# Optimization experiments

Measured on AMD Instinct MI355X. Metric: run time of the kernel, lower is better.

## Reference

```python
import jax, jax.numpy as jnp
import numpy as np

EPS = 1e-5
PDIM, QKD, DIM = 64, 16, 256
SCALE = QKD ** -0.5


def setup_inputs() -> dict:
    key = jax.random.key(0)
    ks = jax.random.split(key, 13)
    B, H, W = 8, 64, 64
    return {
        "x": jax.random.normal(ks[0], (B, DIM, H, W), jnp.float32),
        "gn_g": jax.random.uniform(ks[1], (PDIM,), jnp.float32, 0.5, 1.5),
        "gn_b": jax.random.normal(ks[2], (PDIM,), jnp.float32) * 0.1,
        "qkv_w": jax.random.normal(ks[3], (2 * QKD + PDIM, PDIM), jnp.float32) * (PDIM ** -0.5),
        "qkv_bn_g": jax.random.uniform(ks[4], (2 * QKD + PDIM,), jnp.float32, 0.5, 1.5),
        "qkv_bn_b": jax.random.normal(ks[5], (2 * QKD + PDIM,), jnp.float32) * 0.1,
        "qkv_rm": jax.random.normal(ks[6], (2 * QKD + PDIM,), jnp.float32) * 0.1,
        "qkv_rv": jax.random.uniform(ks[7], (2 * QKD + PDIM,), jnp.float32, 0.5, 1.5),
        "proj_w": jax.random.normal(ks[8], (DIM, DIM), jnp.float32) * (DIM ** -0.5),
        "proj_bn_g": jax.random.uniform(ks[9], (DIM,), jnp.float32, 0.5, 1.5),
        "proj_bn_b": jax.random.normal(ks[10], (DIM,), jnp.float32) * 0.1,
        "proj_rm": jax.random.normal(ks[11], (DIM,), jnp.float32) * 0.1,
        "proj_rv": jax.random.uniform(ks[12], (DIM,), jnp.float32, 0.5, 1.5),
    }


def _bn(y, g, b, rm, rv):
    # inference BatchNorm over channel axis 1 of [B,C,H,W]
    inv = g / jnp.sqrt(rv + EPS)
    return y * inv[None, :, None, None] + (b - rm * inv)[None, :, None, None]


def reference(x, gn_g, gn_b, qkv_w, qkv_bn_g, qkv_bn_b, qkv_rm, qkv_rv,
              proj_w, proj_bn_g, proj_bn_b, proj_rm, proj_rv):
    B, C, H, W = x.shape
    x1, x2 = x[:, :PDIM], x[:, PDIM:]
    # GroupNorm with 1 group: normalize over (C,H,W) per sample
    mu = jnp.mean(x1, axis=(1, 2, 3), keepdims=True)
    var = jnp.var(x1, axis=(1, 2, 3), keepdims=True)
    x1n = (x1 - mu) / jnp.sqrt(var + EPS)
    x1n = x1n * gn_g[None, :, None, None] + gn_b[None, :, None, None]
    # qkv: 1x1 conv + BN
    qkv = jnp.einsum('bchw,oc->bohw', x1n, qkv_w)
    qkv = _bn(qkv, qkv_bn_g, qkv_bn_b, qkv_rm, qkv_rv)
    q, k, v = qkv[:, :QKD], qkv[:, QKD:2 * QKD], qkv[:, 2 * QKD:]
    N = H * W
    q = q.reshape(B, QKD, N)
    k = k.reshape(B, QKD, N)
    v = v.reshape(B, PDIM, N)
    attn = jnp.einsum('bcn,bcm->bnm', q, k) * SCALE  # [B,N,N]
    attn = jax.nn.softmax(attn, axis=-1)
    x1_attn = jnp.einsum('bcm,bnm->bcn', v, attn).reshape(B, PDIM, H, W)
    xc = jnp.concatenate([x1_attn, x2], axis=1)
    # proj: ReLU -> 1x1 conv -> BN
    y = jnp.einsum('bchw,oc->bohw', jax.nn.relu(xc), proj_w)
    return _bn(y, proj_bn_g, proj_bn_b, proj_rm, proj_rv)
```

## Files before the change

### kernel.cpp

```cpp
#include <hip/hip_runtime.h>
#include <hip/hip_bf16.h>

typedef __bf16 bf16;
typedef __bf16 bf16x4 __attribute__((ext_vector_type(4)));
typedef __bf16 bf16x8 __attribute__((ext_vector_type(8)));
typedef float  f32x16 __attribute__((ext_vector_type(16)));

#define MFMA32 __builtin_amdgcn_mfma_f32_32x32x16_bf16
#define EPSV 1e-5f
#define QSCALE 0.36067376022224085f

__device__ __forceinline__ f32x16 fzero16() {
  f32x16 z;
#pragma unroll
  for (int i = 0; i < 16; ++i) z[i] = 0.f;
  return z;
}

__global__ __launch_bounds__(256) void k_stats_partial(const float* __restrict__ x,
                                                       float* __restrict__ part) {
  const int b = blockIdx.x >> 5, k = blockIdx.x & 31;
  const float* p = x + (size_t)b * 256 * 4096 + k * 8192;
  const int t = threadIdx.x;
  float s = 0.f, q = 0.f;
#pragma unroll
  for (int j = 0; j < 8; ++j) {
    float4 v = ((const float4*)p)[t + j * 256];
    s += v.x + v.y + v.z + v.w;
    q += v.x * v.x + v.y * v.y + v.z * v.z + v.w * v.w;
  }
  __shared__ float ls[256], lq[256];
  ls[t] = s; lq[t] = q;
  __syncthreads();
  for (int off = 128; off > 0; off >>= 1) {
    if (t < off) { ls[t] += ls[t + off]; lq[t] += lq[t + off]; }
    __syncthreads();
  }
  if (t == 0) { part[blockIdx.x * 2] = ls[0]; part[blockIdx.x * 2 + 1] = lq[0]; }
}

__global__ __launch_bounds__(256) void k_stats_final(const float* __restrict__ part,
                                                     float* __restrict__ stats) {
  const int t = threadIdx.x, b = t >> 5, k = t & 31;
  float s = part[(b * 32 + k) * 2], q = part[(b * 32 + k) * 2 + 1];
  for (int off = 16; off > 0; off >>= 1) {
    s += __shfl_down(s, off, 32);
    q += __shfl_down(q, off, 32);
  }
  if (k == 0) {
    const float inv_n = 1.f / 262144.f;
    const float mu = s * inv_n;
    const float var = q * inv_n - mu * mu;
    stats[b * 2] = mu;
    stats[b * 2 + 1] = rsqrtf(var + EPSV);
  }
}

__global__ __launch_bounds__(256) void k_qkv(
    const float* __restrict__ x, const float* __restrict__ gn_g, const float* __restrict__ gn_b,
    const float* __restrict__ qkv_w, const float* __restrict__ bn_g, const float* __restrict__ bn_b,
    const float* __restrict__ bn_rm, const float* __restrict__ bn_rv,
    const float* __restrict__ stats,
    bf16* __restrict__ qw, bf16* __restrict__ kw, bf16* __restrict__ vw) {
  const int b = blockIdx.x >> 6, tile = blockIdx.x & 63;
  const int n0 = tile * 64, t = threadIdx.x;
  __shared__ float xn[64][68];
  __shared__ float W[64][96];
  __shared__ float beta_s[96];
  const float mu = stats[b * 2], rstd = stats[b * 2 + 1];
  {
    const int c = t >> 2, f = t & 3;
    const float A = rstd * gn_g[c], B = gn_b[c] - mu * A;
    const float* xr = x + ((size_t)b * 256 + c) * 4096 + n0;
#pragma unroll
    for (int j = 0; j < 4; ++j) {
      float4 v = ((const float4*)xr)[f * 4 + j];
      const int nb = f * 16 + j * 4;
      xn[c][nb + 0] = v.x * A + B; xn[c][nb + 1] = v.y * A + B;
      xn[c][nb + 2] = v.z * A + B; xn[c][nb + 3] = v.w * A + B;
    }
  }
  for (int oc = t; oc < 96 * 8; oc += 256) {
    const int o = oc >> 3, ch = (oc & 7) * 8;
    const float inv = bn_g[o] * rsqrtf(bn_rv[o] + EPSV);
    if (ch == 0) beta_s[o] = bn_b[o] - bn_rm[o] * inv;
    const float* wr = qkv_w + o * 64 + ch;
#pragma unroll
    for (int i = 0; i < 8; ++i) W[ch + i][o] = wr[i] * inv;
  }
  __syncthreads();
  const int o_l = t & 31, ng = t >> 5;
#pragma unroll 1
  for (int p = 0; p < 3; ++p) {
    const int o = p * 32 + o_l;
    float acc[8];
#pragma unroll
    for (int j = 0; j < 8; ++j) acc[j] = 0.f;
    for (int c = 0; c < 64; ++c) {
      const float wv = W[c][o];
      const float* xr = &xn[c][ng * 8];
#pragma unroll
      for (int j = 0; j < 8; ++j) acc[j] += wv * xr[j];
    }
    const float beta = beta_s[o];
    const int nb = n0 + ng * 8;
    if (p == 0) {
      if (o < 16) {
#pragma unroll
        for (int j = 0; j < 8; ++j)
          qw[((size_t)b * 4096 + nb + j) * 16 + o] = (bf16)((acc[j] + beta) * QSCALE);
      } else {
#pragma unroll
        for (int j = 0; j < 8; ++j)
          kw[((size_t)b * 4096 + nb + j) * 16 + (o - 16)] = (bf16)(acc[j] + beta);
      }
    } else {
      const int c = (p - 1) * 32 + o_l;
      const int IT = nb >> 5;
      const int m4 = nb & 31;
      const int f  = ((m4 >> 4) << 1) + (c >> 5);
      const int b3 = (m4 >> 3) & 1;
      char* base = (char*)vw + (size_t)b * 524288 + (size_t)IT * 4096 +
                   f * 1024 + (c & 31) * 16 + b3 * 8;
      bf16x4 pk0, pk1;
#pragma unroll
      for (int i = 0; i < 4; ++i) {
        pk0[i] = (bf16)(acc[i] + beta);
        pk1[i] = (bf16)(acc[4 + i] + beta);
      }
      *(bf16x4*)base = pk0;
      *(bf16x4*)(base + 512) = pk1;
    }
  }
}

__global__ __launch_bounds__(256, 4) void k_attn(
    const bf16* __restrict__ qw, const bf16* __restrict__ kw,
    const bf16* __restrict__ vw, const float* __restrict__ x,
    bf16* __restrict__ xc) {
  __shared__ __align__(16) char smem[16896];
  const int orig = blockIdx.x;
  const int wg = (orig & 7) * 128 + (orig >> 3);
  const int b = wg >> 7, qblk = wg & 127;
  const int t = threadIdx.x;
  const int wid = t >> 6, l = t & 63, ln = l & 31, g = l >> 5;
  const int m0 = wid * 1024;

  const bf16* qb = qw + (size_t)b * 4096 * 16;
  const char* kb = (const char*)(kw + (size_t)b * 4096 * 16);
  const char* vfb = (const char*)vw + (size_t)b * 524288;

  const char* kptr = kb + (size_t)(m0 + ln) * 32 + 16 * g;
  const char* vptr = vfb + (size_t)(m0 >> 5) * 4096 + l * 16;

  const int nq = qblk * 32 + ln;
  const bf16x8 qf = *(const bf16x8*)(qb + (size_t)nq * 16 + g * 8);

  f32x16 O0 = fzero16(), O1 = fzero16();
  float l_run = 0.f;

  uint4 kcA = *(const uint4*)kptr;
  uint4 kcB = *(const uint4*)(kptr + 1024);
  uint4 va0 = *(const uint4*)(vptr);
  uint4 vb0 = *(const uint4*)(vptr + 1024);
  uint4 va1 = *(const uint4*)(vptr + 2048);
  uint4 vb1 = *(const uint4*)(vptr + 3072);

#pragma unroll 2
  for (int it = 0; it < 32; ++it) {
    uint4 kn, wa0, wb0, wa1, wb1;
    if (it + 2 < 32) kn = *(const uint4*)(kptr + (it + 2) * 1024);
    if (it + 1 < 32) {
      wa0 = *(const uint4*)(vptr + (it + 1) * 4096);
      wb0 = *(const uint4*)(vptr + (it + 1) * 4096 + 1024);
      wa1 = *(const uint4*)(vptr + (it + 1) * 4096 + 2048);
      wb1 = *(const uint4*)(vptr + (it + 1) * 4096 + 3072);
    }
    f32x16 S = MFMA32(__builtin_bit_cast(bf16x8, kcA), qf, fzero16(), 0, 0, 0);
    float ts = 0.f;
#pragma unroll
    for (int r = 0; r < 16; ++r) { S[r] = __builtin_amdgcn_exp2f(S[r]); ts += S[r]; }
    ts += __shfl_xor(ts, 32, 64);
    l_run += ts;
    bf16x8 pb0, pb1;
#pragma unroll
    for (int r = 0; r < 8; ++r) { pb0[r] = (bf16)S[r]; pb1[r] = (bf16)S[r + 8]; }
    O0 = MFMA32(__builtin_bit_cast(bf16x8, va0), pb0, O0, 0, 0, 0);
    O1 = MFMA32(__builtin_bit_cast(bf16x8, vb0), pb0, O1, 0, 0, 0);
    O0 = MFMA32(__builtin_bit_cast(bf16x8, va1), pb1, O0, 0, 0, 0);
    O1 = MFMA32(__builtin_bit_cast(bf16x8, vb1), pb1, O1, 0, 0, 0);
    kcA = kcB; kcB = kn;
    va0 = wa0; vb0 = wb0; va1 = wa1; vb1 = wb1;
  }

  {
    char* orow = smem + wid * 4096 + ln * 128;
    const int msk = 2 * (ln & 7);
#pragma unroll
    for (int h = 0; h < 2; ++h) {
      const f32x16& O = h ? O1 : O0;
#pragma unroll
      for (int j = 0; j < 4; ++j) {
        bf16x4 e;
#pragma unroll
        for (int i = 0; i < 4; ++i) e[i] = (bf16)O[4 * j + i];
        const int chunk = h * 8 + 2 * j + g;
        *(bf16x4*)(orow + ((chunk ^ msk) << 3)) = e;
      }
    }
    if (g == 0) *(float*)(smem + 16384 + wid * 128 + ln * 4) = l_run;
  }
  __syncthreads();

  {
    const int n = t >> 3, k8 = t & 7;
    const int off = ((2 * k8) ^ (2 * (n & 7))) << 3;
    float L = 0.f;
    float acc[8];
#pragma unroll
    for (int e = 0; e < 8; ++e) acc[e] = 0.f;
#pragma unroll
    for (int kr_ = 0; kr_ < 4; ++kr_) {
      L += *(const float*)(smem + 16384 + kr_ * 128 + n * 4);
      const bf16x8 v = *(const bf16x8*)(smem + kr_ * 4096 + n * 128 + off);
#pragma unroll
      for (int e = 0; e < 8; ++e) acc[e] += (float)v[e];
    }
    const float rL = 1.0f / L;
    bf16x8 o8;
#pragma unroll
    for (int e = 0; e < 8; ++e) o8[e] = (bf16)fmaxf(acc[e] * rL, 0.f);
    *(bf16x8*)(xc + ((size_t)b * 4096 + qblk * 32 + n) * 256 + k8 * 8) = o8;
  }
  __syncthreads();

  {
    unsigned* tile_u = (unsigned*)smem;
    const float* xb = x + ((size_t)b * 256 + 64) * 4096 + qblk * 32;
#pragma unroll
    for (int i = 0; i < 3; ++i) {
      const int idx = i * 256 + t;
      const int cp = idx >> 3, f = idx & 7;
      const float4 a = *(const float4*)(xb + (size_t)(2 * cp) * 4096 + f * 4);
      const float4 c4 = *(const float4*)(xb + (size_t)(2 * cp + 1) * 4096 + f * 4);
      const float av[4] = {a.x, a.y, a.z, a.w};
      const float cv[4] = {c4.x, c4.y, c4.z, c4.w};
#pragma unroll
      for (int e = 0; e < 4; ++e) {
        const unsigned u =
            (unsigned)__builtin_bit_cast(unsigned short, (bf16)fmaxf(av[e], 0.f)) |
            ((unsigned)__builtin_bit_cast(unsigned short, (bf16)fmaxf(cv[e], 0.f)) << 16);
        tile_u[(f * 4 + e) * 97 + cp] = u;
      }
    }
    __syncthreads();
#pragma unroll
    for (int i = 0; i < 3; ++i) {
      const int idx = i * 256 + t;
      const int n = idx / 24, q = idx % 24;
      const uint4 d = *(const uint4*)&tile_u[n * 97 + q * 4];
      *(uint4*)(xc + ((size_t)b * 4096 + qblk * 32 + n) * 256 + 64 + q * 8) = d;
    }
  }
}

__global__ __launch_bounds__(256, 2) void k_proj(
    const bf16* __restrict__ xc, const float* __restrict__ pw,
    const float* __restrict__ bn_g, const float* __restrict__ bn_b,
    const float* __restrict__ bn_rm, const float* __restrict__ bn_rv,
    float* __restrict__ out) {
  const int orig = blockIdx.x;
  const int wg = (orig & 7) * 64 + (orig >> 3);
  const int b = wg >> 6, rem = wg & 63, nt = rem >> 1, oh = rem & 1;
  const int n0 = nt * 128, o0 = oh * 128;
  const int t = threadIdx.x, w = t >> 6, l = t & 63, ln = l & 31, g = l >> 5;

  __shared__ __align__(16) bf16 pws[128 * 256];
  __shared__ float beta_s[128];

  {
    const int o = t >> 1, half = t & 1;
    const float inv = bn_g[o0 + o] * rsqrtf(bn_rv[o0 + o] + EPSV);
    if (half == 0) beta_s[o] = bn_b[o0 + o] - bn_rm[o0 + o] * inv;
    const float* wr = pw + (size_t)(o0 + o) * 256 + half * 128;
    const int s_hh = (o & 15) * 8;
#pragma unroll
    for (int j = 0; j < 16; ++j) {
      const float4 a = ((const float4*)wr)[j * 2];
      const float4 c4 = ((const float4*)wr)[j * 2 + 1];
      bf16x8 v8;
      v8[0] = (bf16)(a.x * inv);  v8[1] = (bf16)(a.y * inv);
      v8[2] = (bf16)(a.z * inv);  v8[3] = (bf16)(a.w * inv);
      v8[4] = (bf16)(c4.x * inv); v8[5] = (bf16)(c4.y * inv);
      v8[6] = (bf16)(c4.z * inv); v8[7] = (bf16)(c4.w * inv);
      *(bf16x8*)&pws[o * 256 + ((half * 128 + j * 8) ^ s_hh)] = v8;
    }
  }
  __syncthreads();

  const bf16* xrow = xc + ((size_t)b * 4096 + n0 + w * 32 + ln) * 256;
  const int sw = (ln & 15) * 8;
  f32x16 acc0 = fzero16(), acc1 = fzero16(), acc2 = fzero16(), acc3 = fzero16();
#pragma unroll 4
  for (int ck = 0; ck < 256; ck += 16) {
    const bf16x8 bfrag = *(const bf16x8*)(xrow + ck + g * 8);
    const int cidx = (ck + g * 8) ^ sw;
    const bf16x8 a0 = *(const bf16x8*)&pws[(ln) * 256 + cidx];
    const bf16x8 a1 = *(const bf16x8*)&pws[(32 + ln) * 256 + cidx];
    const bf16x8 a2 = *(const bf16x8*)&pws[(64 + ln) * 256 + cidx];
    const bf16x8 a3 = *(const bf16x8*)&pws[(96 + ln) * 256 + cidx];
    acc0 = MFMA32(a0, bfrag, acc0, 0, 0, 0);
    acc1 = MFMA32(a1, bfrag, acc1, 0, 0, 0);
    acc2 = MFMA32(a2, bfrag, acc2, 0, 0, 0);
    acc3 = MFMA32(a3, bfrag, acc3, 0, 0, 0);
  }
  const int ncol = n0 + w * 32 + ln;
  float* ob = out + (size_t)b * 256 * 4096 + ncol;
#pragma unroll
  for (int og = 0; og < 4; ++og) {
    const f32x16& A = og == 0 ? acc0 : og == 1 ? acc1 : og == 2 ? acc2 : acc3;
#pragma unroll
    for (int r = 0; r < 16; ++r) {
      const int o_loc = og * 32 + (r & 3) + 8 * (r >> 2) + 4 * g;
      ob[(size_t)(o0 + o_loc) * 4096] = A[r] + beta_s[o_loc];
    }
  }
}

extern "C" void kernel_launch(void* const* d_in, const int* in_sizes, int n_in,
                              void* d_out, int out_size, void* d_ws, size_t ws_size,
                              hipStream_t stream) {
  (void)in_sizes; (void)n_in; (void)out_size; (void)ws_size;
  const float* x        = (const float*)d_in[0];
  const float* gn_g     = (const float*)d_in[1];
  const float* gn_b     = (const float*)d_in[2];
  const float* qkv_w    = (const float*)d_in[3];
  const float* qkv_bn_g = (const float*)d_in[4];
  const float* qkv_bn_b = (const float*)d_in[5];
  const float* qkv_rm   = (const float*)d_in[6];
  const float* qkv_rv   = (const float*)d_in[7];
  const float* proj_w   = (const float*)d_in[8];
  const float* proj_bn_g = (const float*)d_in[9];
  const float* proj_bn_b = (const float*)d_in[10];
  const float* proj_rm  = (const float*)d_in[11];
  const float* proj_rv  = (const float*)d_in[12];

  char* ws = (char*)d_ws;
  float* part  = (float*)ws;
  float* stats = (float*)(ws + 4096);
  bf16* qw = (bf16*)(ws + 8192);
  bf16* kw = (bf16*)(ws + 8192 + (1u << 20));
  bf16* vw = (bf16*)(ws + 8192 + (2u << 20));
  bf16* xc = (bf16*)(ws + 8192 + (6u << 20));

  k_stats_partial<<<256, 256, 0, stream>>>(x, part);
  k_stats_final<<<1, 256, 0, stream>>>(part, stats);
  k_qkv<<<512, 256, 0, stream>>>(x, gn_g, gn_b, qkv_w, qkv_bn_g, qkv_bn_b,
                                 qkv_rm, qkv_rv, stats, qw, kw, vw);
  k_attn<<<1024, 256, 0, stream>>>(qw, kw, vw, x, xc);
  k_proj<<<512, 256, 0, stream>>>(xc, proj_w, proj_bn_g, proj_bn_b,
                                  proj_rm, proj_rv, (float*)d_out);
}
```

Baseline: 86.99 us.

## Stream K/V tiles into LDS via async global_load_lds double-buffered ring

Replaces register-prefetched K and V global loads in the attention loop with direct global-to-LDS DMA into a per-wave two-slot ring, using explicit vmcnt/lgkmcnt waits. Tiles are then read back from LDS each iteration. The per-iteration cross-half shuffle of the row sum is moved out of the loop to a single shuffle at the end. This aims to cut register pressure and load latency stalls, but raises LDS use to 40KB per block, which may lower occupancy at the 4-blocks-per-CU launch bound.

```diff
diff --git a/kernel.cpp b/kernel.cpp
--- a/kernel.cpp
+++ b/kernel.cpp
@@ -15,6 +15,12 @@
 #pragma unroll
   for (int i = 0; i < 16; ++i) z[i] = 0.f;
   return z;
+}
+
+__device__ __forceinline__ void dma16(const void* g, void* s) {
+  __builtin_amdgcn_global_load_lds(
+      (const __attribute__((address_space(1))) void*)g,
+      (__attribute__((address_space(3))) void*)s, 16, 0, 0);
 }
 
 __global__ __launch_bounds__(256) void k_stats_partial(const float* __restrict__ x,
@@ -138,7 +144,7 @@
     const bf16* __restrict__ qw, const bf16* __restrict__ kw,
     const bf16* __restrict__ vw, const float* __restrict__ x,
     bf16* __restrict__ xc) {
-  __shared__ __align__(16) char smem[16896];
+  __shared__ __align__(16) char smem[40960];
   const int orig = blockIdx.x;
   const int wg = (orig & 7) * 128 + (orig >> 3);
   const int b = wg >> 7, qblk = wg & 127;
@@ -150,48 +156,66 @@
   const char* kb = (const char*)(kw + (size_t)b * 4096 * 16);
   const char* vfb = (const char*)vw + (size_t)b * 524288;
 
-  const char* kptr = kb + (size_t)(m0 + ln) * 32 + 16 * g;
-  const char* vptr = vfb + (size_t)(m0 >> 5) * 4096 + l * 16;
+  const char* kdma = kb + (size_t)m0 * 32 + (2 * ln + g) * 16;
+  const char* vdma = vfb + (size_t)(m0 >> 5) * 4096 + l * 16;
+  char* ring = smem + wid * 10240;
 
   const int nq = qblk * 32 + ln;
   const bf16x8 qf = *(const bf16x8*)(qb + (size_t)nq * 16 + g * 8);
+  asm volatile("" :: "v"(qf));
 
   f32x16 O0 = fzero16(), O1 = fzero16();
   float l_run = 0.f;
 
-  uint4 kcA = *(const uint4*)kptr;
-  uint4 kcB = *(const uint4*)(kptr + 1024);
-  uint4 va0 = *(const uint4*)(vptr);
-  uint4 vb0 = *(const uint4*)(vptr + 1024);
-  uint4 va1 = *(const uint4*)(vptr + 2048);
-  uint4 vb1 = *(const uint4*)(vptr + 3072);
-
-#pragma unroll 2
+#pragma unroll
+  for (int pt = 0; pt < 2; ++pt) {
+    char* dst = ring + pt * 5120;
+    const char* ks = kdma + (size_t)pt * 1024;
+    const char* vs = vdma + (size_t)pt * 4096;
+    dma16(ks, dst);
+    dma16(vs, dst + 1024);
+    dma16(vs + 1024, dst + 2048);
+    dma16(vs + 2048, dst + 3072);
+    dma16(vs + 3072, dst + 4096);
+  }
+
+#pragma unroll 1
   for (int it = 0; it < 32; ++it) {
-    uint4 kn, wa0, wb0, wa1, wb1;
-    if (it + 2 < 32) kn = *(const uint4*)(kptr + (it + 2) * 1024);
-    if (it + 1 < 32) {
-      wa0 = *(const uint4*)(vptr + (it + 1) * 4096);
-      wb0 = *(const uint4*)(vptr + (it + 1) * 4096 + 1024);
-      wa1 = *(const uint4*)(vptr + (it + 1) * 4096 + 2048);
-      wb1 = *(const uint4*)(vptr + (it + 1) * 4096 + 3072);
-    }
-    f32x16 S = MFMA32(__builtin_bit_cast(bf16x8, kcA), qf, fzero16(), 0, 0, 0);
+    if (it < 31) { asm volatile("s_waitcnt vmcnt(5)" ::: "memory"); }
+    else         { asm volatile("s_waitcnt vmcnt(0)" ::: "memory"); }
+    const char* rb = ring + (it & 1) * 5120 + l * 16;
+    const uint4 kc = *(const uint4*)rb;
+    const uint4 v0 = *(const uint4*)(rb + 1024);
+    const uint4 v1 = *(const uint4*)(rb + 2048);
+    const uint4 v2 = *(const uint4*)(rb + 3072);
+    const uint4 v3 = *(const uint4*)(rb + 4096);
+    f32x16 S = MFMA32(__builtin_bit_cast(bf16x8, kc), qf, fzero16(), 0, 0, 0);
     float ts = 0.f;
 #pragma unroll
     for (int r = 0; r < 16; ++r) { S[r] = __builtin_amdgcn_exp2f(S[r]); ts += S[r]; }
-    ts += __shfl_xor(ts, 32, 64);
     l_run += ts;
     bf16x8 pb0, pb1;
 #pragma unroll
     for (int r = 0; r < 8; ++r) { pb0[r] = (bf16)S[r]; pb1[r] = (bf16)S[r + 8]; }
-    O0 = MFMA32(__builtin_bit_cast(bf16x8, va0), pb0, O0, 0, 0, 0);
-    O1 = MFMA32(__builtin_bit_cast(bf16x8, vb0), pb0, O1, 0, 0, 0);
-    O0 = MFMA32(__builtin_bit_cast(bf16x8, va1), pb1, O0, 0, 0, 0);
-    O1 = MFMA32(__builtin_bit_cast(bf16x8, vb1), pb1, O1, 0, 0, 0);
-    kcA = kcB; kcB = kn;
-    va0 = wa0; vb0 = wb0; va1 = wa1; vb1 = wb1;
-  }
+    O0 = MFMA32(__builtin_bit_cast(bf16x8, v0), pb0, O0, 0, 0, 0);
+    O1 = MFMA32(__builtin_bit_cast(bf16x8, v1), pb0, O1, 0, 0, 0);
+    O0 = MFMA32(__builtin_bit_cast(bf16x8, v2), pb1, O0, 0, 0, 0);
+    O1 = MFMA32(__builtin_bit_cast(bf16x8, v3), pb1, O1, 0, 0, 0);
+    asm volatile("s_waitcnt lgkmcnt(0)" ::: "memory");
+    if (it + 2 < 32) {
+      char* dst = ring + (it & 1) * 5120;
+      const char* ks = kdma + (size_t)(it + 2) * 1024;
+      const char* vs = vdma + (size_t)(it + 2) * 4096;
+      dma16(ks, dst);
+      dma16(vs, dst + 1024);
+      dma16(vs + 1024, dst + 2048);
+      dma16(vs + 2048, dst + 3072);
+      dma16(vs + 3072, dst + 4096);
+    }
+  }
+  l_run += __shfl_xor(l_run, 32, 64);
+
+  __syncthreads();
 
   {
     char* orow = smem + wid * 4096 + ln * 128;
```

After: 90.53 us. +4.1%, slower.
